# Performance work log

Hardware: AMD Instinct MI355X
Metric: run time of the kernel (lower is better)

## Reference

```python
import jax, jax.numpy as jnp
import numpy as np

B, H, I, E, K = 512, 1024, 1024, 32, 4
EPS, ALPHA, LIMIT = 1e-5, 1.702, 7.0


def _swiglu(h):
    # interleaved split: even cols -> glu path, odd cols -> linear path
    x_glu = jnp.minimum(h[..., ::2], LIMIT)
    x_lin = jnp.clip(h[..., 1::2], -LIMIT, LIMIT)
    return x_glu * jax.nn.sigmoid(ALPHA * x_glu) * (x_lin + 1.0)


def setup_inputs() -> dict:
    key = jax.random.key(0)
    ks = jax.random.split(key, 7)
    n = lambda k, shape, s: jax.random.normal(k, shape, dtype=jnp.float32) * s
    return {
        "x": n(ks[0], (B, H), 1.0),
        "norm_scale": jnp.ones((H,), jnp.float32),
        "gate_w": n(ks[1], (E, H), 0.02),
        "gate_b": n(ks[2], (E,), 0.02),
        "mlp1_w": n(ks[3], (E, 2 * I, H), 0.02),
        "mlp1_b": n(ks[4], (E, 2 * I), 0.02),
        "mlp2_w": n(ks[5], (E, H, I), 0.02),
        "mlp2_b": n(ks[6], (E, H), 0.02),
    }


def reference(x, norm_scale, gate_w, gate_b, mlp1_w, mlp1_b, mlp2_w, mlp2_b):
    # RMSNorm in fp32
    t = x * jax.lax.rsqrt(jnp.mean(x * x, axis=-1, keepdims=True) + EPS) * norm_scale
    # gate + top-k routing; softmax over the k selected logits
    g = t @ gate_w.T + gate_b                      # [B, E]
    vals, idx = jax.lax.top_k(g, K)                # [B, K]
    w = jax.nn.softmax(vals, axis=-1)              # [B, K]
    # dense routing weights [B, E]: w_dense[b, e] = sum_k w[b,k] * (idx[b,k]==e)
    w_dense = jnp.zeros((t.shape[0], gate_w.shape[0]), t.dtype)
    w_dense = w_dense.at[jnp.arange(t.shape[0])[:, None], idx].add(w)
    # grouped-dense equivalent of the per-token gathered einsum:
    # original: einsum('beck,bk->bec', mlp1_w[idx], t); here we compute all
    # experts densely and combine with w_dense (zero for unselected experts),
    # which is the same math without materializing [B,K,2I,H] weights.
    h = jnp.einsum('bk,eck->bec', t, mlp1_w) + mlp1_b   # [B, E, 2I]
    a = _swiglu(h)                                       # [B, E, I]
    o = jnp.einsum('bei,ehi->beh', a, mlp2_w) + mlp2_b   # [B, E, H]
    y = jnp.einsum('beh,be->bh', o, w_dense)             # [B, H]
    return x + y
```

## Files before the change

### kernel.cpp

```cpp
#include <hip/hip_runtime.h>
#include <hip/hip_bf16.h>
#include <math.h>


#define NB   512
#define NH   1024
#define NI   1024
#define NE   32
#define NK   4
#define N2I  2048
#define CAP  512
#define PADK 40

static constexpr float EPS   = 1e-5f;
static constexpr float ALPHA = 1.702f;
static constexpr float LIMIT = 7.0f;

typedef short bf16x8 __attribute__((ext_vector_type(8)));
typedef float f32x4  __attribute__((ext_vector_type(4)));

__device__ __forceinline__ short hi16(float x) {
    return (short)(__float_as_uint(x) >> 16);
}
__device__ __forceinline__ short lo16(float x) {
    unsigned hb = __float_as_uint(x) & 0xFFFF0000u;
    float r = x - __uint_as_float(hb);
    return (short)(__float_as_uint(r) >> 16);
}
__device__ __forceinline__ short rne16(float x) {
    unsigned u = __float_as_uint(x);
    return (short)((u + 0x7FFFu + ((u >> 16) & 1u)) >> 16);
}
__device__ __forceinline__ void cvtsplit8(float4 v0, float4 v1,
                                          bf16x8& hh, bf16x8& ll) {
    float f[8] = {v0.x, v0.y, v0.z, v0.w, v1.x, v1.y, v1.z, v1.w};
#pragma unroll
    for (int i = 0; i < 8; i++) { hh[i] = hi16(f[i]); ll[i] = lo16(f[i]); }
}
__device__ __forceinline__ void cvtrne8(float4 v0, float4 v1, bf16x8& hh) {
    float f[8] = {v0.x, v0.y, v0.z, v0.w, v1.x, v1.y, v1.z, v1.w};
#pragma unroll
    for (int i = 0; i < 8; i++) hh[i] = rne16(f[i]);
}

__global__ __launch_bounds__(256) void k_rms_gate(
    const float* __restrict__ x, const float* __restrict__ scale,
    const float* __restrict__ gw, const float* __restrict__ gb,
    float* __restrict__ t, int* __restrict__ cnt,
    int* __restrict__ tok, int* __restrict__ tke, float* __restrict__ tkw) {
    __shared__ float sh_t[NH];
    __shared__ float sh_red[4];
    __shared__ float sh_g[NE];
    const int b = blockIdx.x, tid = threadIdx.x;
    const int lane = tid & 63, wid = tid >> 6;

    float4 xv = reinterpret_cast<const float4*>(x + (size_t)b * NH)[tid];
    float ss = xv.x * xv.x + xv.y * xv.y + xv.z * xv.z + xv.w * xv.w;
#pragma unroll
    for (int o = 32; o >= 1; o >>= 1) ss += __shfl_down(ss, o);
    if (lane == 0) sh_red[wid] = ss;
    __syncthreads();
    const float tot = sh_red[0] + sh_red[1] + sh_red[2] + sh_red[3];
    const float r = rsqrtf(tot * (1.0f / NH) + EPS);
    float4 sv = reinterpret_cast<const float4*>(scale)[tid];
    float4 tv;
    tv.x = xv.x * r * sv.x; tv.y = xv.y * r * sv.y;
    tv.z = xv.z * r * sv.z; tv.w = xv.w * r * sv.w;
    reinterpret_cast<float4*>(sh_t)[tid] = tv;
    reinterpret_cast<float4*>(t + (size_t)b * NH)[tid] = tv;
    __syncthreads();

#pragma unroll
    for (int q = 0; q < 8; q++) {
        const int e = wid * 8 + q;
        const float* __restrict__ w = gw + (size_t)e * NH;
        float p = 0.f;
#pragma unroll
        for (int i = 0; i < 16; i++) { int k = lane + 64 * i; p += sh_t[k] * w[k]; }
#pragma unroll
        for (int o = 32; o >= 1; o >>= 1) p += __shfl_down(p, o);
        if (lane == 0) sh_g[e] = p + gb[e];
    }
    __syncthreads();

    if (tid == 0) {
        float gv[NE];
#pragma unroll
        for (int e = 0; e < NE; e++) gv[e] = sh_g[e];
        float vals[NK]; int ids[NK];
#pragma unroll
        for (int k = 0; k < NK; k++) {
            int bi = 0; float bv = gv[0];
            for (int e = 1; e < NE; e++) if (gv[e] > bv) { bv = gv[e]; bi = e; }
            vals[k] = bv; ids[k] = bi; gv[bi] = -1e30f;
        }
        const float m = vals[0];
        float s = 0.f, wv[NK];
#pragma unroll
        for (int k = 0; k < NK; k++) { wv[k] = __expf(vals[k] - m); s += wv[k]; }
        const float inv = 1.f / s;
#pragma unroll
        for (int k = 0; k < NK; k++) {
            const int e = ids[k];
            const int pos = atomicAdd(&cnt[e], 1);
            tok[e * CAP + pos] = b;
            tke[b * NK + k] = (e << 16) | pos;
            tkw[b * NK + k] = wv[k] * inv;
        }
    }
}

__global__ void k_prefix(const int* __restrict__ cnt, int* __restrict__ base) {
    if (threadIdx.x == 0) {
        int r = 0;
        for (int e = 0; e < NE; e++) { base[e] = r; r += cnt[e]; }
    }
}

#define LOADBUF(Aa, Ab, Ac, Ad, Ba, Bb, Bc, Bd, k)                           \
    do {                                                                     \
        Aa = *(const float4*)(asrc + (k));      Ab = *(const float4*)(asrc + (k) + 4);  \
        Ac = *(const float4*)(asrc + (k) + 16); Ad = *(const float4*)(asrc + (k) + 20); \
        Ba = *(const float4*)(bsrc + (k));      Bb = *(const float4*)(bsrc + (k) + 4);  \
        Bc = *(const float4*)(bsrc + (k) + 16); Bd = *(const float4*)(bsrc + (k) + 20); \
    } while (0)

#define CVT_STORE(Aa, Ab, Ac, Ad, Ba, Bb, Bc, Bd)                            \
    do {                                                                     \
        bf16x8 hh, ll;                                                       \
        cvtsplit8(Aa, Ab, hh, ll);                                           \
        if (zA) { hh = (bf16x8)(short)0; ll = (bf16x8)(short)0; }            \
        *(bf16x8*)&Ah[srow][sh8] = hh;  *(bf16x8*)&Al[srow][sh8] = ll;       \
        cvtsplit8(Ac, Ad, hh, ll);                                           \
        if (zA) { hh = (bf16x8)(short)0; ll = (bf16x8)(short)0; }            \
        *(bf16x8*)&Ah[srow][sh8 + 16] = hh; *(bf16x8*)&Al[srow][sh8 + 16] = ll; \
        cvtrne8(Ba, Bb, hh);  *(bf16x8*)&Bh[srow][sh8] = hh;                 \
        cvtrne8(Bc, Bd, hh);  *(bf16x8*)&Bh[srow][sh8 + 16] = hh;            \
    } while (0)

#define MFMA_PHASE()                                                         \
    do {                                                                     \
        bf16x8 ah[4], al[4], bh[4];                                          \
        _Pragma("unroll")                                                    \
        for (int m = 0; m < 4; m++) {                                        \
            const int r = wr * 64 + m * 16 + frow;                           \
            ah[m] = *(const bf16x8*)&Ah[r][fk];                              \
            al[m] = *(const bf16x8*)&Al[r][fk];                              \
        }                                                                    \
        _Pragma("unroll")                                                    \
        for (int n = 0; n < 4; n++) {                                        \
            const int c = wc * 64 + n * 16 + frow;                           \
            bh[n] = *(const bf16x8*)&Bh[c][fk];                              \
        }                                                                    \
        _Pragma("unroll")                                                    \
        for (int m = 0; m < 4; m++)                                          \
            _Pragma("unroll")                                                \
            for (int n = 0; n < 4; n++) {                                    \
                acc[m][n] = __builtin_amdgcn_mfma_f32_16x16x32_bf16(ah[m], bh[n], acc[m][n], 0, 0, 0); \
                acc[m][n] = __builtin_amdgcn_mfma_f32_16x16x32_bf16(al[m], bh[n], acc[m][n], 0, 0, 0); \
            }                                                                \
    } while (0)

__global__ __launch_bounds__(256, 2) void k_mlp1(
    const float* __restrict__ t, const float* __restrict__ w1,
    const float* __restrict__ b1, const int* __restrict__ cnt,
    const int* __restrict__ base, const int* __restrict__ tok,
    float* __restrict__ a) {
    const int e  = blockIdx.z;
    const int ne = cnt[e];
    const int m0 = blockIdx.y * 128;
    if (m0 >= ne) return;
    const int c0 = blockIdx.x * 128;
    const float* __restrict__ W = w1 + (size_t)e * N2I * NH + (size_t)c0 * NH;

    __shared__ short Ah[128][PADK], Al[128][PADK], Bh[128][PADK];
    __shared__ int   toks[128];

    const int tid = threadIdx.x;
    if (tid < 128) toks[tid] = (m0 + tid < ne) ? tok[e * CAP + m0 + tid] : -1;
    __syncthreads();

    const int lane = tid & 63;
    const int wid  = tid >> 6;
    const int wr = wid >> 1, wc = wid & 1;
    const int frow = lane & 15;
    const int fk   = (lane >> 4) * 8;
    const int srow = tid >> 1;
    const int sh8  = (tid & 1) * 8;

    f32x4 acc[4][4] = {};

    const int tka = toks[srow];
    const bool zA = (tka < 0);
    const float* __restrict__ asrc = t + (size_t)(zA ? 0 : tka) * NH + sh8;
    const float* __restrict__ bsrc = W + (size_t)srow * NH + sh8;

    float4 A0a, A0b, A0c, A0d, B0a, B0b, B0c, B0d;
    float4 A1a, A1b, A1c, A1d, B1a, B1b, B1c, B1d;
    LOADBUF(A0a, A0b, A0c, A0d, B0a, B0b, B0c, B0d, 0);
    LOADBUF(A1a, A1b, A1c, A1d, B1a, B1b, B1c, B1d, 32);

    for (int k0 = 0; k0 < NH; k0 += 64) {
        CVT_STORE(A0a, A0b, A0c, A0d, B0a, B0b, B0c, B0d);
        if (k0 + 64 < NH)
            LOADBUF(A0a, A0b, A0c, A0d, B0a, B0b, B0c, B0d, k0 + 64);
        __syncthreads();
        MFMA_PHASE();
        __syncthreads();
        CVT_STORE(A1a, A1b, A1c, A1d, B1a, B1b, B1c, B1d);
        if (k0 + 96 < NH)
            LOADBUF(A1a, A1b, A1c, A1d, B1a, B1b, B1c, B1d, k0 + 96);
        __syncthreads();
        MFMA_PHASE();
        __syncthreads();
    }

    const int slot0 = base[e];
#pragma unroll
    for (int m = 0; m < 4; m++)
#pragma unroll
        for (int n = 0; n < 4; n++) {
            const int gcol = c0 + wc * 64 + n * 16 + frow;
            const float bias = b1[e * N2I + gcol];
            f32x4 v = acc[m][n];
#pragma unroll
            for (int j = 0; j < 4; j++) {
                const float h  = v[j] + bias;
                const float hp = __shfl_xor(h, 1);
                const int row = m0 + wr * 64 + m * 16 + (lane >> 4) * 4 + j;
                if (!(lane & 1) && row < ne) {
                    const float xg = fminf(h, LIMIT);
                    const float xl = fminf(fmaxf(hp, -LIMIT), LIMIT);
                    const float sg2 = 1.f / (1.f + __expf(-ALPHA * xg));
                    a[(size_t)(slot0 + row) * NI + (gcol >> 1)] = xg * sg2 * (xl + 1.f);
                }
            }
        }
}

__global__ __launch_bounds__(256, 2) void k_mlp2(
    const float* __restrict__ a, const float* __restrict__ w2,
    const float* __restrict__ b2, const int* __restrict__ cnt,
    const int* __restrict__ base, float* __restrict__ o) {
    const int e  = blockIdx.z;
    const int ne = cnt[e];
    const int m0 = blockIdx.y * 128;
    if (m0 >= ne) return;
    const int c0 = blockIdx.x * 128;
    const int slot0 = base[e];
    const float* __restrict__ W = w2 + (size_t)e * NH * NI + (size_t)c0 * NI;

    __shared__ short Ah[128][PADK], Al[128][PADK], Bh[128][PADK];

    const int tid = threadIdx.x;
    const int lane = tid & 63;
    const int wid  = tid >> 6;
    const int wr = wid >> 1, wc = wid & 1;
    const int frow = lane & 15;
    const int fk   = (lane >> 4) * 8;
    const int srow = tid >> 1;
    const int sh8  = (tid & 1) * 8;

    f32x4 acc[4][4] = {};

    const bool zA = (m0 + srow >= ne);
    const float* __restrict__ asrc =
        a + (size_t)(zA ? 0 : (slot0 + m0 + srow)) * NI + sh8;
    const float* __restrict__ bsrc = W + (size_t)srow * NI + sh8;

    float4 A0a, A0b, A0c, A0d, B0a, B0b, B0c, B0d;
    float4 A1a, A1b, A1c, A1d, B1a, B1b, B1c, B1d;
    LOADBUF(A0a, A0b, A0c, A0d, B0a, B0b, B0c, B0d, 0);
    LOADBUF(A1a, A1b, A1c, A1d, B1a, B1b, B1c, B1d, 32);

    for (int k0 = 0; k0 < NI; k0 += 64) {
        CVT_STORE(A0a, A0b, A0c, A0d, B0a, B0b, B0c, B0d);
        if (k0 + 64 < NI)
            LOADBUF(A0a, A0b, A0c, A0d, B0a, B0b, B0c, B0d, k0 + 64);
        __syncthreads();
        MFMA_PHASE();
        __syncthreads();
        CVT_STORE(A1a, A1b, A1c, A1d, B1a, B1b, B1c, B1d);
        if (k0 + 96 < NI)
            LOADBUF(A1a, A1b, A1c, A1d, B1a, B1b, B1c, B1d, k0 + 96);
        __syncthreads();
        MFMA_PHASE();
        __syncthreads();
    }

#pragma unroll
    for (int m = 0; m < 4; m++)
#pragma unroll
        for (int n = 0; n < 4; n++) {
            const int gcol = c0 + wc * 64 + n * 16 + frow;
            const float bias = b2[e * NH + gcol];
            f32x4 v = acc[m][n];
#pragma unroll
            for (int j = 0; j < 4; j++) {
                const int row = m0 + wr * 64 + m * 16 + (lane >> 4) * 4 + j;
                if (row < ne)
                    o[(size_t)(slot0 + row) * NH + gcol] = v[j] + bias;
            }
        }
}

__global__ __launch_bounds__(256) void k_combine(
    const float* __restrict__ x, const float* __restrict__ o,
    const int* __restrict__ base, const int* __restrict__ tke,
    const float* __restrict__ tkw, float* __restrict__ out) {
    const int b = blockIdx.x, tid = threadIdx.x;
    int slots[NK]; float wk[NK];
#pragma unroll
    for (int k = 0; k < NK; k++) {
        const int v = tke[b * NK + k];
        slots[k] = base[v >> 16] + (v & 0xFFFF);
        wk[k] = tkw[b * NK + k];
    }
    float4 r = reinterpret_cast<const float4*>(x + (size_t)b * NH)[tid];
#pragma unroll
    for (int k = 0; k < NK; k++) {
        float4 ov = reinterpret_cast<const float4*>(o + (size_t)slots[k] * NH)[tid];
        r.x += wk[k] * ov.x; r.y += wk[k] * ov.y;
        r.z += wk[k] * ov.z; r.w += wk[k] * ov.w;
    }
    reinterpret_cast<float4*>(out + (size_t)b * NH)[tid] = r;
}

extern "C" void kernel_launch(void* const* d_in, const int* in_sizes, int n_in,
                              void* d_out, int out_size, void* d_ws, size_t ws_size,
                              hipStream_t stream) {
    const float* x     = (const float*)d_in[0];
    const float* scale = (const float*)d_in[1];
    const float* gw    = (const float*)d_in[2];
    const float* gb    = (const float*)d_in[3];
    const float* w1    = (const float*)d_in[4];
    const float* b1    = (const float*)d_in[5];
    const float* w2    = (const float*)d_in[6];
    const float* b2    = (const float*)d_in[7];
    float* out = (float*)d_out;

    float* t   = (float*)d_ws;
    float* a   = t + (size_t)NB * NH;
    float* o   = a + (size_t)NB * NK * NI;
    int*   tok = (int*)(o + (size_t)NB * NK * NH);
    int*   tke = tok + NE * CAP;
    float* tkw = (float*)(tke + NB * NK);
    int*   cnt = (int*)(tkw + NB * NK);
    int*   bse = cnt + NE;

    hipMemsetAsync(cnt, 0, NE * sizeof(int), stream);
    k_rms_gate<<<NB, 256, 0, stream>>>(x, scale, gw, gb, t, cnt, tok, tke, tkw);
    k_prefix<<<1, 64, 0, stream>>>(cnt, bse);
    k_mlp1<<<dim3(N2I / 128, NB / 128, NE), 256, 0, stream>>>(t, w1, b1, cnt, bse, tok, a);
    k_mlp2<<<dim3(NH / 128, NB / 128, NE), 256, 0, stream>>>(a, w2, b2, cnt, bse, o);
    k_combine<<<NB, 256, 0, stream>>>(x, o, bse, tke, tkw, out);
}
```

Baseline: 594.0 us.

## Fuse combine into mlp2 via atomics, double-buffer LDS, drop prefix kernel

The combine and prefix kernels are removed. mlp2 now scatters routing-weighted outputs directly into the output with float atomicAdd, and the rms kernel pre-writes the residual x into the output. Each block computes the expert slot offset inline from cnt. The GEMM k-loops switch to double-buffered shared memory with one barrier per half-step, overlapping the convert-and-store of the next tile with MFMA on the current one. This cuts two launches, the intermediate o buffer round trip and one of two barriers per phase, at the cost of doubled LDS (possible occupancy loss), atomic contention, and nondeterministic summation order.

After: 627.2 us. 5.6% more time.

```diff
diff --git a/kernel.cpp b/kernel.cpp
--- a/kernel.cpp
+++ b/kernel.cpp
@@ -47,7 +47,8 @@
     const float* __restrict__ x, const float* __restrict__ scale,
     const float* __restrict__ gw, const float* __restrict__ gb,
     float* __restrict__ t, int* __restrict__ cnt,
-    int* __restrict__ tok, int* __restrict__ tke, float* __restrict__ tkw) {
+    int* __restrict__ tok, float* __restrict__ wte,
+    float* __restrict__ out) {
     __shared__ float sh_t[NH];
     __shared__ float sh_red[4];
     __shared__ float sh_g[NE];
@@ -55,6 +56,7 @@
     const int lane = tid & 63, wid = tid >> 6;
 
     float4 xv = reinterpret_cast<const float4*>(x + (size_t)b * NH)[tid];
+    reinterpret_cast<float4*>(out + (size_t)b * NH)[tid] = xv;
     float ss = xv.x * xv.x + xv.y * xv.y + xv.z * xv.z + xv.w * xv.w;
 #pragma unroll
     for (int o = 32; o >= 1; o >>= 1) ss += __shfl_down(ss, o);
@@ -104,16 +106,8 @@
             const int e = ids[k];
             const int pos = atomicAdd(&cnt[e], 1);
             tok[e * CAP + pos] = b;
-            tke[b * NK + k] = (e << 16) | pos;
-            tkw[b * NK + k] = wv[k] * inv;
+            wte[e * CAP + pos] = wv[k] * inv;
         }
-    }
-}
-
-__global__ void k_prefix(const int* __restrict__ cnt, int* __restrict__ base) {
-    if (threadIdx.x == 0) {
-        int r = 0;
-        for (int e = 0; e < NE; e++) { base[e] = r; r += cnt[e]; }
     }
 }
 
@@ -125,32 +119,32 @@
         Bc = *(const float4*)(bsrc + (k) + 16); Bd = *(const float4*)(bsrc + (k) + 20); \
     } while (0)
 
-#define CVT_STORE(Aa, Ab, Ac, Ad, Ba, Bb, Bc, Bd)                            \
+#define CVT_STORE(S, Aa, Ab, Ac, Ad, Ba, Bb, Bc, Bd)                         \
     do {                                                                     \
         bf16x8 hh, ll;                                                       \
         cvtsplit8(Aa, Ab, hh, ll);                                           \
         if (zA) { hh = (bf16x8)(short)0; ll = (bf16x8)(short)0; }            \
-        *(bf16x8*)&Ah[srow][sh8] = hh;  *(bf16x8*)&Al[srow][sh8] = ll;       \
+        *(bf16x8*)&Ah[S][srow][sh8] = hh;  *(bf16x8*)&Al[S][srow][sh8] = ll; \
         cvtsplit8(Ac, Ad, hh, ll);                                           \
         if (zA) { hh = (bf16x8)(short)0; ll = (bf16x8)(short)0; }            \
-        *(bf16x8*)&Ah[srow][sh8 + 16] = hh; *(bf16x8*)&Al[srow][sh8 + 16] = ll; \
-        cvtrne8(Ba, Bb, hh);  *(bf16x8*)&Bh[srow][sh8] = hh;                 \
-        cvtrne8(Bc, Bd, hh);  *(bf16x8*)&Bh[srow][sh8 + 16] = hh;            \
+        *(bf16x8*)&Ah[S][srow][sh8 + 16] = hh; *(bf16x8*)&Al[S][srow][sh8 + 16] = ll; \
+        cvtrne8(Ba, Bb, hh);  *(bf16x8*)&Bh[S][srow][sh8] = hh;              \
+        cvtrne8(Bc, Bd, hh);  *(bf16x8*)&Bh[S][srow][sh8 + 16] = hh;         \
     } while (0)
 
-#define MFMA_PHASE()                                                         \
+#define MFMA_PHASE(S)                                                        \
     do {                                                                     \
         bf16x8 ah[4], al[4], bh[4];                                          \
         _Pragma("unroll")                                                    \
         for (int m = 0; m < 4; m++) {                                        \
             const int r = wr * 64 + m * 16 + frow;                           \
-            ah[m] = *(const bf16x8*)&Ah[r][fk];                              \
-            al[m] = *(const bf16x8*)&Al[r][fk];                              \
+            ah[m] = *(const bf16x8*)&Ah[S][r][fk];                           \
+            al[m] = *(const bf16x8*)&Al[S][r][fk];                           \
         }                                                                    \
         _Pragma("unroll")                                                    \
         for (int n = 0; n < 4; n++) {                                        \
             const int c = wc * 64 + n * 16 + frow;                           \
-            bh[n] = *(const bf16x8*)&Bh[c][fk];                              \
+            bh[n] = *(const bf16x8*)&Bh[S][c][fk];                           \
         }                                                                    \
         _Pragma("unroll")                                                    \
         for (int m = 0; m < 4; m++)                                          \
@@ -161,11 +155,28 @@
             }                                                                \
     } while (0)
 
+#define DBUF_KLOOP(KDIM)                                                     \
+    LOADBUF(A0a, A0b, A0c, A0d, B0a, B0b, B0c, B0d, 0);                      \
+    LOADBUF(A1a, A1b, A1c, A1d, B1a, B1b, B1c, B1d, 32);                     \
+    CVT_STORE(0, A0a, A0b, A0c, A0d, B0a, B0b, B0c, B0d);                    \
+    for (int k0 = 0; k0 < (KDIM); k0 += 64) {                                \
+        __syncthreads();                                                     \
+        if (k0 + 64 < (KDIM))                                                \
+            LOADBUF(A0a, A0b, A0c, A0d, B0a, B0b, B0c, B0d, k0 + 64);        \
+        CVT_STORE(1, A1a, A1b, A1c, A1d, B1a, B1b, B1c, B1d);                \
+        MFMA_PHASE(0);                                                       \
+        __syncthreads();                                                     \
+        if (k0 + 96 < (KDIM))                                                \
+            LOADBUF(A1a, A1b, A1c, A1d, B1a, B1b, B1c, B1d, k0 + 96);        \
+        if (k0 + 64 < (KDIM))                                                \
+            CVT_STORE(0, A0a, A0b, A0c, A0d, B0a, B0b, B0c, B0d);            \
+        MFMA_PHASE(1);                                                       \
+    }
+
 __global__ __launch_bounds__(256, 2) void k_mlp1(
     const float* __restrict__ t, const float* __restrict__ w1,
     const float* __restrict__ b1, const int* __restrict__ cnt,
-    const int* __restrict__ base, const int* __restrict__ tok,
-    float* __restrict__ a) {
+    const int* __restrict__ tok, float* __restrict__ a) {
     const int e  = blockIdx.z;
     const int ne = cnt[e];
     const int m0 = blockIdx.y * 128;
@@ -173,11 +184,13 @@
     const int c0 = blockIdx.x * 128;
     const float* __restrict__ W = w1 + (size_t)e * N2I * NH + (size_t)c0 * NH;
 
-    __shared__ short Ah[128][PADK], Al[128][PADK], Bh[128][PADK];
+    __shared__ short Ah[2][128][PADK], Al[2][128][PADK], Bh[2][128][PADK];
     __shared__ int   toks[128];
 
     const int tid = threadIdx.x;
     if (tid < 128) toks[tid] = (m0 + tid < ne) ? tok[e * CAP + m0 + tid] : -1;
+    int slot0 = 0;
+    for (int q = 0; q < NE; q++) slot0 += (q < e) ? cnt[q] : 0;
     __syncthreads();
 
     const int lane = tid & 63;
@@ -197,25 +210,8 @@
 
     float4 A0a, A0b, A0c, A0d, B0a, B0b, B0c, B0d;
     float4 A1a, A1b, A1c, A1d, B1a, B1b, B1c, B1d;
-    LOADBUF(A0a, A0b, A0c, A0d, B0a, B0b, B0c, B0d, 0);
-    LOADBUF(A1a, A1b, A1c, A1d, B1a, B1b, B1c, B1d, 32);
-
-    for (int k0 = 0; k0 < NH; k0 += 64) {
-        CVT_STORE(A0a, A0b, A0c, A0d, B0a, B0b, B0c, B0d);
-        if (k0 + 64 < NH)
-            LOADBUF(A0a, A0b, A0c, A0d, B0a, B0b, B0c, B0d, k0 + 64);
-        __syncthreads();
-        MFMA_PHASE();
-        __syncthreads();
-        CVT_STORE(A1a, A1b, A1c, A1d, B1a, B1b, B1c, B1d);
-        if (k0 + 96 < NH)
-            LOADBUF(A1a, A1b, A1c, A1d, B1a, B1b, B1c, B1d, k0 + 96);
-        __syncthreads();
-        MFMA_PHASE();
-        __syncthreads();
-    }
-
-    const int slot0 = base[e];
+    DBUF_KLOOP(NH);
+
 #pragma unroll
     for (int m = 0; m < 4; m++)
 #pragma unroll
@@ -241,18 +237,29 @@
 __global__ __launch_bounds__(256, 2) void k_mlp2(
     const float* __restrict__ a, const float* __restrict__ w2,
     const float* __restrict__ b2, const int* __restrict__ cnt,
-    const int* __restrict__ base, float* __restrict__ o) {
+    const int* __restrict__ tok, const float* __restrict__ wte,
+    float* __restrict__ out) {
     const int e  = blockIdx.z;
     const int ne = cnt[e];
     const int m0 = blockIdx.y * 128;
     if (m0 >= ne) return;
     const int c0 = blockIdx.x * 128;
-    const int slot0 = base[e];
     const float* __restrict__ W = w2 + (size_t)e * NH * NI + (size_t)c0 * NI;
 
-    __shared__ short Ah[128][PADK], Al[128][PADK], Bh[128][PADK];
+    __shared__ short Ah[2][128][PADK], Al[2][128][PADK], Bh[2][128][PADK];
+    __shared__ int   toks[128];
+    __shared__ float wts[128];
 
     const int tid = threadIdx.x;
+    if (tid < 128) {
+        const bool v = (m0 + tid < ne);
+        toks[tid] = v ? tok[e * CAP + m0 + tid] : -1;
+        wts[tid]  = v ? wte[e * CAP + m0 + tid] : 0.f;
+    }
+    int slot0 = 0;
+    for (int q = 0; q < NE; q++) slot0 += (q < e) ? cnt[q] : 0;
+    __syncthreads();
+
     const int lane = tid & 63;
     const int wid  = tid >> 6;
     const int wr = wid >> 1, wc = wid & 1;
@@ -270,23 +277,7 @@
 
     float4 A0a, A0b, A0c, A0d, B0a, B0b, B0c, B0d;
     float4 A1a, A1b, A1c, A1d, B1a, B1b, B1c, B1d;
-    LOADBUF(A0a, A0b, A0c, A0d, B0a, B0b, B0c, B0d, 0);
-    LOADBUF(A1a, A1b, A1c, A1d, B1a, B1b, B1c, B1d, 32);
-
-    for (int k0 = 0; k0 < NI; k0 += 64) {
-        CVT_STORE(A0a, A0b, A0c, A0d, B0a, B0b, B0c, B0d);
-        if (k0 + 64 < NI)
-            LOADBUF(A0a, A0b, A0c, A0d, B0a, B0b, B0c, B0d, k0 + 64);
-        __syncthreads();
-        MFMA_PHASE();
-        __syncthreads();
-        CVT_STORE(A1a, A1b, A1c, A1d, B1a, B1b, B1c, B1d);
-        if (k0 + 96 < NI)
-            LOADBUF(A1a, A1b, A1c, A1d, B1a, B1b, B1c, B1d, k0 + 96);
-        __syncthreads();
-        MFMA_PHASE();
-        __syncthreads();
-    }
+    DBUF_KLOOP(NI);
 
 #pragma unroll
     for (int m = 0; m < 4; m++)
@@ -297,33 +288,14 @@
             f32x4 v = acc[m][n];
 #pragma unroll
             for (int j = 0; j < 4; j++) {
-                const int row = m0 + wr * 64 + m * 16 + (lane >> 4) * 4 + j;
-                if (row < ne)
-                    o[(size_t)(slot0 + row) * NH + gcol] = v[j] + bias;
+                const int row = wr * 64 + m * 16 + (lane >> 4) * 4 + j;
+                if (m0 + row < ne) {
+                    const int   tk = toks[row];
+                    const float wv = wts[row];
+                    atomicAdd(&out[(size_t)tk * NH + gcol], wv * (v[j] + bias));
+                }
             }
         }
-}
-
-__global__ __launch_bounds__(256) void k_combine(
-    const float* __restrict__ x, const float* __restrict__ o,
-    const int* __restrict__ base, const int* __restrict__ tke,
-    const float* __restrict__ tkw, float* __restrict__ out) {
-    const int b = blockIdx.x, tid = threadIdx.x;
-    int slots[NK]; float wk[NK];
-#pragma unroll
-    for (int k = 0; k < NK; k++) {
-        const int v = tke[b * NK + k];
-        slots[k] = base[v >> 16] + (v & 0xFFFF);
-        wk[k] = tkw[b * NK + k];
-    }
-    float4 r = reinterpret_cast<const float4*>(x + (size_t)b * NH)[tid];
-#pragma unroll
-    for (int k = 0; k < NK; k++) {
-        float4 ov = reinterpret_cast<const float4*>(o + (size_t)slots[k] * NH)[tid];
-        r.x += wk[k] * ov.x; r.y += wk[k] * ov.y;
-        r.z += wk[k] * ov.z; r.w += wk[k] * ov.w;
-    }
-    reinterpret_cast<float4*>(out + (size_t)b * NH)[tid] = r;
 }
 
 extern "C" void kernel_launch(void* const* d_in, const int* in_sizes, int n_in,
@@ -341,17 +313,12 @@
 
     float* t   = (float*)d_ws;
     float* a   = t + (size_t)NB * NH;
-    float* o   = a + (size_t)NB * NK * NI;
-    int*   tok = (int*)(o + (size_t)NB * NK * NH);
-    int*   tke = tok + NE * CAP;
-    float* tkw = (float*)(tke + NB * NK);
-    int*   cnt = (int*)(tkw + NB * NK);
-    int*   bse = cnt + NE;
+    int*   tok = (int*)(a + (size_t)NB * NK * NI);
+    float* wte = (float*)(tok + NE * CAP);
+    int*   cnt = (int*)(wte + NE * CAP);
 
     hipMemsetAsync(cnt, 0, NE * sizeof(int), stream);
-    k_rms_gate<<<NB, 256, 0, stream>>>(x, scale, gw, gb, t, cnt, tok, tke, tkw);
-    k_prefix<<<1, 64, 0, stream>>>(cnt, bse);
-    k_mlp1<<<dim3(N2I / 128, NB / 128, NE), 256, 0, stream>>>(t, w1, b1, cnt, bse, tok, a);
-    k_mlp2<<<dim3(NH / 128, NB / 128, NE), 256, 0, stream>>>(a, w2, b2, cnt, bse, o);
-    k_combine<<<NB, 256, 0, stream>>>(x, o, bse, tke, tkw, out);
-}
+    k_rms_gate<<<NB, 256, 0, stream>>>(x, scale, gw, gb, t, cnt, tok, wte, out);
+    k_mlp1<<<dim3(N2I / 128, NB / 128, NE), 256, 0, stream>>>(t, w1, b1, cnt, tok, a);
+    k_mlp2<<<dim3(NH / 128, NB / 128, NE), 256, 0, stream>>>(a, w2, b2, cnt, tok, wte, out);
+}
```
